# Kernel tuning notes

Measured on AMD Instinct MI355X. Metric: run time of the kernel, lower is better.

## Reference

```python
import jax, jax.numpy as jnp
import numpy as np

D_MODEL = 768
N_HEADS = 12
D_K = D_MODEL // N_HEADS


def setup_inputs() -> dict:
    key = jax.random.key(0)
    kq, kk, kv, kwq, kbq, kwo, kbo = jax.random.split(key, 7)
    B, S = 1, 4096
    s = 1.0 / np.sqrt(D_MODEL)
    return {
        "q": jax.random.normal(kq, (B, S, D_MODEL), jnp.float32),
        "k": jax.random.normal(kk, (B, S, D_MODEL), jnp.float32),
        "v": jax.random.normal(kv, (B, S, D_MODEL), jnp.float32),
        # nn.Linear weights stored as [out, in]; note the original forward
        # uses W_q for Q, K, AND V (W_k/W_v are never used), so only W_q and
        # W_o are materialized here.
        "Wq": jax.random.uniform(kwq, (D_MODEL, D_MODEL), jnp.float32, -s, s),
        "bq": jax.random.uniform(kbq, (D_MODEL,), jnp.float32, -s, s),
        "Wo": jax.random.uniform(kwo, (D_MODEL, D_MODEL), jnp.float32, -s, s),
        "bo": jax.random.uniform(kbo, (D_MODEL,), jnp.float32, -s, s),
    }


def _split_heads(x):  # [B,S,D] -> [B,H,S,Dk]
    B, S, _ = x.shape
    return x.reshape(B, S, N_HEADS, D_K).transpose(0, 2, 1, 3)


def reference(q, k, v, Wq, bq, Wo, bo):
    # Faithful to source: same W_q projection applied to q, k, v.
    Q = _split_heads(q @ Wq.T + bq)
    K = _split_heads(k @ Wq.T + bq)
    V = _split_heads(v @ Wq.T + bq)
    scale = 1.0 / np.sqrt(D_K).astype(np.float32)
    scores = jnp.einsum("bhqd,bhkd->bhqk", Q, K) * scale  # [B,H,S,S]
    probs = jax.nn.softmax(scores, axis=-1)
    atten = jnp.einsum("bhqk,bhkd->bhqd", probs, V)
    B, _, S, _ = atten.shape
    concat = atten.transpose(0, 2, 1, 3).reshape(B, S, D_MODEL)
    return concat @ Wo.T + bo
```

## Files before the change

### kernel.cpp

```cpp
#include <hip/hip_runtime.h>
#include <stdint.h>
#include <math.h>


#define SQ 4096
#define DM 768
#define NH 12

typedef float f32x4 __attribute__((ext_vector_type(4)));
typedef short bf16x8 __attribute__((ext_vector_type(8)));
typedef unsigned int u32x4 __attribute__((ext_vector_type(4)));
typedef unsigned short ushort_t;

static __device__ __forceinline__ ushort_t f2bf(float f) {
    unsigned int u = __builtin_bit_cast(unsigned int, f);
    u += 0x7fffu + ((u >> 16) & 1u);
    return (ushort_t)(u >> 16);
}

static __device__ __forceinline__ unsigned int cvt_pk_bf16(float a, float b) {
    unsigned int d;
    asm("v_cvt_pk_bf16_f32 %0, %1, %2" : "=v"(d) : "v"(a), "v"(b));
    return d;
}

static __device__ __forceinline__ float exp2_hw(float x) {
    float r;
    asm("v_exp_f32 %0, %1" : "=v"(r) : "v"(x));
    return r;
}

static __device__ __forceinline__ void gload16(const ushort_t* g, ushort_t* l) {
    __builtin_amdgcn_global_load_lds(
        reinterpret_cast<const __attribute__((address_space(1))) unsigned int*>(
            reinterpret_cast<uintptr_t>(g)),
        reinterpret_cast<__attribute__((address_space(3))) unsigned int*>(
            reinterpret_cast<uintptr_t>(l)),
        16, 0, 0);
}

#define WAITV8 do { asm volatile("s_waitcnt vmcnt(8)" ::: "memory"); \
                    __builtin_amdgcn_sched_barrier(0); } while (0)
#define WAITV0 do { asm volatile("s_waitcnt vmcnt(0)" ::: "memory"); \
                    __builtin_amdgcn_sched_barrier(0); } while (0)

__global__ __launch_bounds__(256) void cvt_all(
    const float* __restrict__ q, const float* __restrict__ k,
    const float* __restrict__ v, const float* __restrict__ Wq,
    const float* __restrict__ Wo, ushort_t* __restrict__ xb,
    ushort_t* __restrict__ wqb, ushort_t* __restrict__ wob) {
    const int NE4 = (SQ * DM) / 4;
    const int NW4 = (DM * DM) / 4;
    int i = blockIdx.x * 256 + threadIdx.x;
    const float* src;
    ushort_t* dst;
    if (i < NE4) { src = q; dst = xb; }
    else if (i < 2 * NE4) { src = k; dst = xb + SQ * DM; i -= NE4; }
    else if (i < 3 * NE4) { src = v; dst = xb + 2 * SQ * DM; i -= 2 * NE4; }
    else if (i < 3 * NE4 + NW4) { src = Wq; dst = wqb; i -= 3 * NE4; }
    else if (i < 3 * NE4 + 2 * NW4) { src = Wo; dst = wob; i -= 3 * NE4 + NW4; }
    else return;
    float4 x = reinterpret_cast<const float4*>(src)[i];
    ushort4 o;
    o.x = f2bf(x.x); o.y = f2bf(x.y); o.z = f2bf(x.z); o.w = f2bf(x.w);
    reinterpret_cast<ushort4*>(dst)[i] = o;
}

template <int EPI>
__global__ __launch_bounds__(256) void gemm_bf16(
    const ushort_t* __restrict__ A, const ushort_t* __restrict__ B,
    const float* __restrict__ bias, ushort_t* __restrict__ proj,
    ushort_t* __restrict__ vt, float* __restrict__ outf) {
    __shared__ __align__(16) ushort_t lsA[128 * 64];
    __shared__ __align__(16) ushort_t lsB[128 * 64];
    const int tid = threadIdx.x;
    const int lane = tid & 63;
    const int w = tid >> 6;
    const int wm = w >> 1, wn = w & 1;
    const int g = lane >> 4, li = lane & 15;
    const int NB = (EPI == 2) ? 32 : 6;
    const int bm = blockIdx.x / NB, bn = blockIdx.x % NB;
    const int arow = bm * 128, brow = bn * 128;
    const int sr = lane >> 3;
    const int sc = ((lane & 7) ^ sr) * 8;

    f32x4 acc[4][4] = {};

    for (int kt = 0; kt < 12; ++kt) {
        const int k0 = kt * 64;
        __syncthreads();
#pragma unroll
        for (int c = 0; c < 4; ++c) {
            const int chunk = w * 4 + c;
            const int r = chunk * 8 + sr;
            gload16(A + (size_t)(arow + r) * DM + k0 + sc, lsA + chunk * 512);
            gload16(B + (size_t)(brow + r) * DM + k0 + sc, lsB + chunk * 512);
        }
        __syncthreads();

        bf16x8 af[4][2];
#pragma unroll
        for (int mf = 0; mf < 4; ++mf) {
            const int row = wm * 64 + mf * 16 + li;
#pragma unroll
            for (int ks = 0; ks < 2; ++ks)
                af[mf][ks] = *reinterpret_cast<const bf16x8*>(
                    lsA + row * 64 + ((ks * 32 + g * 8) ^ ((li & 7) << 3)));
        }
#pragma unroll
        for (int nf = 0; nf < 4; ++nf) {
            const int row = wn * 64 + nf * 16 + li;
            bf16x8 b0 = *reinterpret_cast<const bf16x8*>(
                lsB + row * 64 + ((g * 8) ^ ((li & 7) << 3)));
            bf16x8 b1 = *reinterpret_cast<const bf16x8*>(
                lsB + row * 64 + ((32 + g * 8) ^ ((li & 7) << 3)));
#pragma unroll
            for (int mf = 0; mf < 4; ++mf) {
                acc[mf][nf] = __builtin_amdgcn_mfma_f32_16x16x32_bf16(af[mf][0], b0, acc[mf][nf], 0, 0, 0);
                acc[mf][nf] = __builtin_amdgcn_mfma_f32_16x16x32_bf16(af[mf][1], b1, acc[mf][nf], 0, 0, 0);
            }
        }
    }

    if (EPI == 0) {
        const float qscale = (arow < 4096) ? 0.18033688011112042f : 1.0f;
#pragma unroll
        for (int nf = 0; nf < 4; ++nf) {
            const int col = brow + wn * 64 + nf * 16 + li;
            const float bv = bias[col];
#pragma unroll
            for (int mf = 0; mf < 4; ++mf) {
                const int row0 = arow + wm * 64 + mf * 16 + g * 4;
#pragma unroll
                for (int r = 0; r < 4; ++r)
                    proj[(size_t)(row0 + r) * DM + col] = f2bf((acc[mf][nf][r] + bv) * qscale);
            }
        }
    } else if (EPI == 2) {
        float bv[4][4];
#pragma unroll
        for (int mf = 0; mf < 4; ++mf)
#pragma unroll
            for (int r = 0; r < 4; ++r)
                bv[mf][r] = bias[arow + wm * 64 + mf * 16 + g * 4 + r];
#pragma unroll
        for (int nf = 0; nf < 4; ++nf) {
            const int j = brow + wn * 64 + nf * 16 + li;
            const int pos = (j & ~31) | ((j & 0xC) << 1) | (((j >> 4) & 1) << 2) | (j & 3);
#pragma unroll
            for (int mf = 0; mf < 4; ++mf) {
                const int row0 = arow + wm * 64 + mf * 16 + g * 4;
#pragma unroll
                for (int r = 0; r < 4; ++r)
                    vt[(size_t)(row0 + r) * SQ + pos] = f2bf(acc[mf][nf][r] + bv[mf][r]);
            }
        }
    } else {
#pragma unroll
        for (int nf = 0; nf < 4; ++nf) {
            const int col = brow + wn * 64 + nf * 16 + li;
            const float bv = bias[col];
#pragma unroll
            for (int mf = 0; mf < 4; ++mf) {
                const int row0 = arow + wm * 64 + mf * 16 + g * 4;
#pragma unroll
                for (int r = 0; r < 4; ++r)
                    outf[(size_t)(row0 + r) * DM + col] = acc[mf][nf][r] + bv;
            }
        }
    }
}

__global__ __launch_bounds__(256) void attn_bf16(
    const ushort_t* __restrict__ qk, const ushort_t* __restrict__ vtb,
    ushort_t* __restrict__ cc) {
    __shared__ __align__(16) ushort_t smem[32768];

    const int tid = threadIdx.x, lane = tid & 63, w = tid >> 6;
    const int g = lane >> 4, li = lane & 15;
    const int logical = (blockIdx.x & 7) * 96 + (blockIdx.x >> 3);
    const int h = logical >> 6, qb = logical & 63;
    const int sr = lane >> 3;
    const int sc = ((lane & 7) ^ sr) * 8;
    const int vdr = lane >> 2;
    const int vsc = ((lane & 3) ^ ((lane >> 3) & 3)) * 8;

    const ushort_t* Kb = qk + (size_t)(4096 + w * 1024) * DM + (size_t)h * 64;
    const ushort_t* Vb = vtb + (size_t)(h * 64) * SQ + w * 1024;

    ushort_t* K0 = smem + w * 8192;
    ushort_t* V0 = K0 + 2048;
    ushort_t* K1 = K0 + 4096;
    ushort_t* V1 = K0 + 6144;

    bf16x8 qf[4][2];
#pragma unroll
    for (int qh = 0; qh < 4; ++qh)
#pragma unroll
        for (int ks = 0; ks < 2; ++ks)
            qf[qh][ks] = *reinterpret_cast<const bf16x8*>(
                qk + (size_t)(qb * 64 + qh * 16 + li) * DM + h * 64 + ks * 32 + g * 8);

    f32x4 oacc[4][5] = {};

    const unsigned int one2 = 0x3F803F80u;
    u32x4 onesu = {one2, one2, one2, one2};
    const bf16x8 vones = __builtin_bit_cast(bf16x8, onesu);

    WAITV0;

#pragma unroll
    for (int c = 0; c < 4; ++c) {
        gload16(Kb + (size_t)(c * 8 + sr) * DM + sc, K0 + c * 512);
        gload16(Vb + (size_t)(c * 16 + vdr) * SQ + vsc, V0 + c * 512);
    }

#define STEP(kp, vp, kn, vn, nxt, DOSTAGE)                                     \
    do {                                                                       \
        if (DOSTAGE) {                                                         \
            const int kvo = (nxt) * 32;                                        \
            _Pragma("unroll") for (int c = 0; c < 4; ++c) {                    \
                gload16(Kb + (size_t)(kvo + c * 8 + sr) * DM + sc,             \
                        (kn) + c * 512);                                       \
                gload16(Vb + (size_t)(c * 16 + vdr) * SQ + kvo + vsc,          \
                        (vn) + c * 512);                                       \
            }                                                                  \
            WAITV8;                                                            \
        } else {                                                               \
            WAITV0;                                                            \
        }                                                                      \
        f32x4 sf[4][2];                                                        \
        _Pragma("unroll") for (int qh = 0; qh < 4; ++qh)                       \
            _Pragma("unroll") for (int nf = 0; nf < 2; ++nf)                   \
                sf[qh][nf] = (f32x4){0.f, 0.f, 0.f, 0.f};                      \
        __builtin_amdgcn_s_setprio(1);                                         \
        _Pragma("unroll") for (int nf = 0; nf < 2; ++nf) {                     \
            const int row = nf * 16 + li;                                      \
            bf16x8 kb0 = *reinterpret_cast<const bf16x8*>(                     \
                (kp) + row * 64 + ((g * 8) ^ ((li & 7) << 3)));                \
            bf16x8 kb1 = *reinterpret_cast<const bf16x8*>(                     \
                (kp) + row * 64 + ((32 + g * 8) ^ ((li & 7) << 3)));           \
            _Pragma("unroll") for (int qh = 0; qh < 4; ++qh) {                 \
                sf[qh][nf] = __builtin_amdgcn_mfma_f32_16x16x32_bf16(          \
                    kb0, qf[qh][0], sf[qh][nf], 0, 0, 0);                      \
                sf[qh][nf] = __builtin_amdgcn_mfma_f32_16x16x32_bf16(          \
                    kb1, qf[qh][1], sf[qh][nf], 0, 0, 0);                      \
            }                                                                  \
        }                                                                      \
        __builtin_amdgcn_s_setprio(0);                                         \
        bf16x8 pa[4];                                                          \
        _Pragma("unroll") for (int qh = 0; qh < 4; ++qh) {                     \
            f32x4 p0, p1;                                                      \
            _Pragma("unroll") for (int r = 0; r < 4; ++r) {                    \
                p0[r] = exp2_hw(sf[qh][0][r]);                                 \
                p1[r] = exp2_hw(sf[qh][1][r]);                                 \
            }                                                                  \
            u32x4 pu;                                                          \
            pu.x = cvt_pk_bf16(p0[0], p0[1]);                                  \
            pu.y = cvt_pk_bf16(p0[2], p0[3]);                                  \
            pu.z = cvt_pk_bf16(p1[0], p1[1]);                                  \
            pu.w = cvt_pk_bf16(p1[2], p1[3]);                                  \
            pa[qh] = __builtin_bit_cast(bf16x8, pu);                           \
        }                                                                      \
        __builtin_amdgcn_s_setprio(1);                                         \
        _Pragma("unroll") for (int nv = 0; nv < 4; ++nv) {                     \
            const int vrow = nv * 16 + li;                                     \
            bf16x8 vb = *reinterpret_cast<const bf16x8*>(                      \
                (vp) + vrow * 32 + ((g ^ ((li >> 1) & 3)) * 8));               \
            _Pragma("unroll") for (int qh = 0; qh < 4; ++qh)                   \
                oacc[qh][nv] = __builtin_amdgcn_mfma_f32_16x16x32_bf16(        \
                    pa[qh], vb, oacc[qh][nv], 0, 0, 0);                        \
        }                                                                      \
        _Pragma("unroll") for (int qh = 0; qh < 4; ++qh)                       \
            oacc[qh][4] = __builtin_amdgcn_mfma_f32_16x16x32_bf16(             \
                pa[qh], vones, oacc[qh][4], 0, 0, 0);                          \
        __builtin_amdgcn_s_setprio(0);                                         \
    } while (0)

#pragma unroll 1
    for (int t = 0; t < 15; ++t) {
        STEP(K0, V0, K1, V1, 2 * t + 1, true);
        STEP(K1, V1, K0, V0, 2 * t + 2, true);
    }
    STEP(K0, V0, K1, V1, 31, true);
    STEP(K1, V1, K0, V0, 32, false);
#undef STEP

    __syncthreads();
    float* ob = reinterpret_cast<float*>(smem);
    if (w > 0) {
        float* base = ob + (w - 1) * 5120;
#pragma unroll
        for (int qh = 0; qh < 4; ++qh)
#pragma unroll
            for (int nv = 0; nv < 5; ++nv)
                *reinterpret_cast<f32x4*>(
                    base + ((qh * 5 + nv) * 64 + lane) * 4) = oacc[qh][nv];
    }
    __syncthreads();
    if (w == 0) {
#pragma unroll
        for (int j = 0; j < 3; ++j) {
            const float* base = ob + j * 5120;
#pragma unroll
            for (int qh = 0; qh < 4; ++qh)
#pragma unroll
                for (int nv = 0; nv < 5; ++nv)
                    oacc[qh][nv] += *reinterpret_cast<const f32x4*>(
                        base + ((qh * 5 + nv) * 64 + lane) * 4);
        }
#pragma unroll
        for (int qh = 0; qh < 4; ++qh) {
            float inv[4];
#pragma unroll
            for (int r = 0; r < 4; ++r) inv[r] = 1.0f / oacc[qh][4][r];
#pragma unroll
            for (int nv = 0; nv < 4; ++nv)
#pragma unroll
                for (int r = 0; r < 4; ++r) {
                    const int row = qb * 64 + qh * 16 + g * 4 + r;
                    const int col = h * 64 + nv * 16 + li;
                    cc[(size_t)row * DM + col] = f2bf(oacc[qh][nv][r] * inv[r]);
                }
        }
    }
}

extern "C" void kernel_launch(void* const* d_in, const int* in_sizes, int n_in,
                              void* d_out, int out_size, void* d_ws, size_t ws_size,
                              hipStream_t stream) {
    const float* q = (const float*)d_in[0];
    const float* k = (const float*)d_in[1];
    const float* v = (const float*)d_in[2];
    const float* Wq = (const float*)d_in[3];
    const float* bq = (const float*)d_in[4];
    const float* Wo = (const float*)d_in[5];
    const float* bo = (const float*)d_in[6];
    float* out = (float*)d_out;

    ushort_t* ws = (ushort_t*)d_ws;
    const int NE = SQ * DM;
    ushort_t* xb = ws;
    ushort_t* wqb = ws + 3 * NE;
    ushort_t* wob = wqb + DM * DM;
    ushort_t* proj = wob + DM * DM;
    ushort_t* vt = proj + 2 * NE;
    ushort_t* cc = vt + NE;

    const int n4 = 3 * (NE / 4) + 2 * ((DM * DM) / 4);
    cvt_all<<<(n4 + 255) / 256, 256, 0, stream>>>(q, k, v, Wq, Wo, xb, wqb, wob);

    gemm_bf16<0><<<(8192 / 128) * 6, 256, 0, stream>>>(xb, wqb, bq, proj, (ushort_t*)nullptr, (float*)nullptr);

    gemm_bf16<2><<<(768 / 128) * 32, 256, 0, stream>>>(wqb, xb + 2 * NE, bq, (ushort_t*)nullptr, vt, (float*)nullptr);

    attn_bf16<<<NH * (SQ / 64), 256, 0, stream>>>(proj, vt, cc);

    gemm_bf16<1><<<(SQ / 128) * 6, 256, 0, stream>>>(cc, wob, bo, (ushort_t*)nullptr, (ushort_t*)nullptr, out);
}
```

Before: 156.5 us.

## Triple-buffer attention KV stages, shrink LDS tiles, merge QK and V projection GEMMs

The attention kernel now stages 16-key K/V tiles into three rotating LDS buffers instead of 32-key tiles in two, splits waits into vmcnt(8)/vmcnt(4), and pairs two 16-key QK blocks per PV MFMA. V is stored with a simpler XOR layout and read as two short4 halves. LDS drops to 48KB with launch_bounds(256,3) so more blocks fit per CU, and the cross-wave reduction becomes a tree. The QK and V projection GEMMs are fused into one 576-block launch to cut a kernel launch. The risks are more register pressure, smaller tiles with more frequent waits, and subtle layout correctness.

```diff
diff --git a/kernel.cpp b/kernel.cpp
--- a/kernel.cpp
+++ b/kernel.cpp
@@ -10,7 +10,10 @@
 typedef float f32x4 __attribute__((ext_vector_type(4)));
 typedef short bf16x8 __attribute__((ext_vector_type(8)));
 typedef unsigned int u32x4 __attribute__((ext_vector_type(4)));
+typedef unsigned int u32x2 __attribute__((ext_vector_type(2)));
 typedef unsigned short ushort_t;
+
+#define MFMA32(a, b, c) __builtin_amdgcn_mfma_f32_16x16x32_bf16((a), (b), (c), 0, 0, 0)
 
 static __device__ __forceinline__ ushort_t f2bf(float f) {
     unsigned int u = __builtin_bit_cast(unsigned int, f);
@@ -41,8 +44,12 @@
 
 #define WAITV8 do { asm volatile("s_waitcnt vmcnt(8)" ::: "memory"); \
                     __builtin_amdgcn_sched_barrier(0); } while (0)
+#define WAITV4 do { asm volatile("s_waitcnt vmcnt(4)" ::: "memory"); \
+                    __builtin_amdgcn_sched_barrier(0); } while (0)
 #define WAITV0 do { asm volatile("s_waitcnt vmcnt(0)" ::: "memory"); \
                     __builtin_amdgcn_sched_barrier(0); } while (0)
+#define WAITLGKM0 do { asm volatile("s_waitcnt lgkmcnt(0)" ::: "memory"); \
+                       __builtin_amdgcn_sched_barrier(0); } while (0)
 
 __global__ __launch_bounds__(256) void cvt_all(
     const float* __restrict__ q, const float* __restrict__ k,
@@ -66,11 +73,10 @@
     reinterpret_cast<ushort4*>(dst)[i] = o;
 }
 
-template <int EPI>
-__global__ __launch_bounds__(256) void gemm_bf16(
-    const ushort_t* __restrict__ A, const ushort_t* __restrict__ B,
-    const float* __restrict__ bias, ushort_t* __restrict__ proj,
-    ushort_t* __restrict__ vt, float* __restrict__ outf) {
+__global__ __launch_bounds__(256) void gemm_qkv(
+    const ushort_t* __restrict__ xb, const ushort_t* __restrict__ wqb,
+    const float* __restrict__ bq, ushort_t* __restrict__ proj,
+    ushort_t* __restrict__ vt) {
     __shared__ __align__(16) ushort_t lsA[128 * 64];
     __shared__ __align__(16) ushort_t lsB[128 * 64];
     const int tid = threadIdx.x;
@@ -78,8 +84,18 @@
     const int w = tid >> 6;
     const int wm = w >> 1, wn = w & 1;
     const int g = lane >> 4, li = lane & 15;
-    const int NB = (EPI == 2) ? 32 : 6;
-    const int bm = blockIdx.x / NB, bn = blockIdx.x % NB;
+    const bool isV = blockIdx.x >= 384;
+    const ushort_t* A;
+    const ushort_t* B;
+    int bm, bn;
+    if (!isV) {
+        A = xb; B = wqb;
+        bm = blockIdx.x / 6; bn = blockIdx.x % 6;
+    } else {
+        A = wqb; B = xb + 2 * SQ * DM;
+        const int b2 = blockIdx.x - 384;
+        bm = b2 / 32; bn = b2 % 32;
+    }
     const int arow = bm * 128, brow = bn * 128;
     const int sr = lane >> 3;
     const int sc = ((lane & 7) ^ sr) * 8;
@@ -116,18 +132,18 @@
                 lsB + row * 64 + ((32 + g * 8) ^ ((li & 7) << 3)));
 #pragma unroll
             for (int mf = 0; mf < 4; ++mf) {
-                acc[mf][nf] = __builtin_amdgcn_mfma_f32_16x16x32_bf16(af[mf][0], b0, acc[mf][nf], 0, 0, 0);
-                acc[mf][nf] = __builtin_amdgcn_mfma_f32_16x16x32_bf16(af[mf][1], b1, acc[mf][nf], 0, 0, 0);
+                acc[mf][nf] = MFMA32(af[mf][0], b0, acc[mf][nf]);
+                acc[mf][nf] = MFMA32(af[mf][1], b1, acc[mf][nf]);
             }
         }
     }
 
-    if (EPI == 0) {
+    if (!isV) {
         const float qscale = (arow < 4096) ? 0.18033688011112042f : 1.0f;
 #pragma unroll
         for (int nf = 0; nf < 4; ++nf) {
             const int col = brow + wn * 64 + nf * 16 + li;
-            const float bv = bias[col];
+            const float bv = bq[col];
 #pragma unroll
             for (int mf = 0; mf < 4; ++mf) {
                 const int row0 = arow + wm * 64 + mf * 16 + g * 4;
@@ -136,17 +152,18 @@
                     proj[(size_t)(row0 + r) * DM + col] = f2bf((acc[mf][nf][r] + bv) * qscale);
             }
         }
-    } else if (EPI == 2) {
+    } else {
         float bv[4][4];
 #pragma unroll
         for (int mf = 0; mf < 4; ++mf)
 #pragma unroll
             for (int r = 0; r < 4; ++r)
-                bv[mf][r] = bias[arow + wm * 64 + mf * 16 + g * 4 + r];
+                bv[mf][r] = bq[arow + wm * 64 + mf * 16 + g * 4 + r];
+        const int xg = (g & 1) << 3;
 #pragma unroll
         for (int nf = 0; nf < 4; ++nf) {
             const int j = brow + wn * 64 + nf * 16 + li;
-            const int pos = (j & ~31) | ((j & 0xC) << 1) | (((j >> 4) & 1) << 2) | (j & 3);
+            const int pos = j ^ xg;
 #pragma unroll
             for (int mf = 0; mf < 4; ++mf) {
                 const int row0 = arow + wm * 64 + mf * 16 + g * 4;
@@ -155,26 +172,80 @@
                     vt[(size_t)(row0 + r) * SQ + pos] = f2bf(acc[mf][nf][r] + bv[mf][r]);
             }
         }
-    } else {
+    }
+}
+
+__global__ __launch_bounds__(256) void gemm_out(
+    const ushort_t* __restrict__ cc, const ushort_t* __restrict__ wob,
+    const float* __restrict__ bo, float* __restrict__ outf) {
+    __shared__ __align__(16) ushort_t lsA[128 * 64];
+    __shared__ __align__(16) ushort_t lsB[128 * 64];
+    const int tid = threadIdx.x;
+    const int lane = tid & 63;
+    const int w = tid >> 6;
+    const int wm = w >> 1, wn = w & 1;
+    const int g = lane >> 4, li = lane & 15;
+    const int bm = blockIdx.x / 6, bn = blockIdx.x % 6;
+    const int arow = bm * 128, brow = bn * 128;
+    const int sr = lane >> 3;
+    const int sc = ((lane & 7) ^ sr) * 8;
+
+    f32x4 acc[4][4] = {};
+
+    for (int kt = 0; kt < 12; ++kt) {
+        const int k0 = kt * 64;
+        __syncthreads();
+#pragma unroll
+        for (int c = 0; c < 4; ++c) {
+            const int chunk = w * 4 + c;
+            const int r = chunk * 8 + sr;
+            gload16(cc + (size_t)(arow + r) * DM + k0 + sc, lsA + chunk * 512);
+            gload16(wob + (size_t)(brow + r) * DM + k0 + sc, lsB + chunk * 512);
+        }
+        __syncthreads();
+
+        bf16x8 af[4][2];
+#pragma unroll
+        for (int mf = 0; mf < 4; ++mf) {
+            const int row = wm * 64 + mf * 16 + li;
+#pragma unroll
+            for (int ks = 0; ks < 2; ++ks)
+                af[mf][ks] = *reinterpret_cast<const bf16x8*>(
+                    lsA + row * 64 + ((ks * 32 + g * 8) ^ ((li & 7) << 3)));
+        }
 #pragma unroll
         for (int nf = 0; nf < 4; ++nf) {
-            const int col = brow + wn * 64 + nf * 16 + li;
-            const float bv = bias[col];
+            const int row = wn * 64 + nf * 16 + li;
+            bf16x8 b0 = *reinterpret_cast<const bf16x8*>(
+                lsB + row * 64 + ((g * 8) ^ ((li & 7) << 3)));
+            bf16x8 b1 = *reinterpret_cast<const bf16x8*>(
+                lsB + row * 64 + ((32 + g * 8) ^ ((li & 7) << 3)));
 #pragma unroll
             for (int mf = 0; mf < 4; ++mf) {
-                const int row0 = arow + wm * 64 + mf * 16 + g * 4;
-#pragma unroll
-                for (int r = 0; r < 4; ++r)
-                    outf[(size_t)(row0 + r) * DM + col] = acc[mf][nf][r] + bv;
+                acc[mf][nf] = MFMA32(af[mf][0], b0, acc[mf][nf]);
+                acc[mf][nf] = MFMA32(af[mf][1], b1, acc[mf][nf]);
             }
         }
     }
-}
-
-__global__ __launch_bounds__(256) void attn_bf16(
+
+#pragma unroll
+    for (int nf = 0; nf < 4; ++nf) {
+        const int col = brow + wn * 64 + nf * 16 + li;
+        const float bv = bo[col];
+#pragma unroll
+        for (int mf = 0; mf < 4; ++mf) {
+            const int row0 = arow + wm * 64 + mf * 16 + g * 4;
+#pragma unroll
+            for (int r = 0; r < 4; ++r)
+                outf[(size_t)(row0 + r) * DM + col] = acc[mf][nf][r] + bv;
+        }
+    }
+}
+
+__global__ __launch_bounds__(256, 3) void attn_bf16(
     const ushort_t* __restrict__ qk, const ushort_t* __restrict__ vtb,
     ushort_t* __restrict__ cc) {
-    __shared__ __align__(16) ushort_t smem[32768];
+    __shared__ __align__(16) ushort_t smem[24576];
 
     const int tid = threadIdx.x, lane = tid & 63, w = tid >> 6;
     const int g = lane >> 4, li = lane & 15;
@@ -182,16 +253,19 @@
     const int h = logical >> 6, qb = logical & 63;
     const int sr = lane >> 3;
     const int sc = ((lane & 7) ^ sr) * 8;
-    const int vdr = lane >> 2;
-    const int vsc = ((lane & 3) ^ ((lane >> 3) & 3)) * 8;
+    const int vd = lane >> 1, vh = lane & 1;
 
     const ushort_t* Kb = qk + (size_t)(4096 + w * 1024) * DM + (size_t)h * 64;
     const ushort_t* Vb = vtb + (size_t)(h * 64) * SQ + w * 1024;
 
-    ushort_t* K0 = smem + w * 8192;
-    ushort_t* V0 = K0 + 2048;
-    ushort_t* K1 = K0 + 4096;
-    ushort_t* V1 = K0 + 6144;
+    ushort_t* base = smem + w * 6144;
+    ushort_t* K0 = base;          ushort_t* V0 = base + 1024;
+    ushort_t* K1 = base + 2048;   ushort_t* V1 = base + 3072;
+    ushort_t* K2 = base + 4096;   ushort_t* V2 = base + 5120;
+
+    const int ko0 = li * 64 + ((g * 8) ^ ((li & 7) << 3));
+    const int ko1 = li * 64 + ((32 + g * 8) ^ ((li & 7) << 3));
+    const int vo = li * 16 + 4 * (g ^ (((li >> 2) & 1) << 1));
 
     bf16x8 qf[4][2];
 #pragma unroll
@@ -202,113 +276,160 @@
                 qk + (size_t)(qb * 64 + qh * 16 + li) * DM + h * 64 + ks * 32 + g * 8);
 
     f32x4 oacc[4][5] = {};
+    u32x2 paA[4];
 
     const unsigned int one2 = 0x3F803F80u;
     u32x4 onesu = {one2, one2, one2, one2};
     const bf16x8 vones = __builtin_bit_cast(bf16x8, onesu);
 
+    auto stage = [&](ushort_t* KT, ushort_t* VT, int kvo) {
+        gload16(Kb + (size_t)(kvo + sr) * DM + sc, KT);
+        gload16(Kb + (size_t)(kvo + 8 + sr) * DM + sc, KT + 512);
+        gload16(Vb + (size_t)vd * SQ + kvo + vh * 8, VT);
+        gload16(Vb + (size_t)(32 + vd) * SQ + kvo + vh * 8, VT + 512);
+    };
+
+    auto qkexp = [&](const ushort_t* KT, f32x4* P) {
+        bf16x8 kb0 = *reinterpret_cast<const bf16x8*>(KT + ko0);
+        bf16x8 kb1 = *reinterpret_cast<const bf16x8*>(KT + ko1);
+        __builtin_amdgcn_s_setprio(1);
+#pragma unroll
+        for (int qh = 0; qh < 4; ++qh) {
+            f32x4 s = {};
+            s = MFMA32(kb0, qf[qh][0], s);
+            s = MFMA32(kb1, qf[qh][1], s);
+            P[qh] = s;
+        }
+        __builtin_amdgcn_s_setprio(0);
+#pragma unroll
+        for (int qh = 0; qh < 4; ++qh) {
+            f32x4 p;
+#pragma unroll
+            for (int r = 0; r < 4; ++r) p[r] = exp2_hw(P[qh][r]);
+            P[qh] = p;
+        }
+    };
+
+    auto pvacc = [&](const ushort_t* VA, const ushort_t* VB, const bf16x8* pa) {
+        __builtin_amdgcn_s_setprio(1);
+#pragma unroll
+        for (int nv = 0; nv < 4; ++nv) {
+            short4 a4 = *reinterpret_cast<const short4*>(VA + vo + nv * 256);
+            short4 b4 = *reinterpret_cast<const short4*>(VB + vo + nv * 256);
+            bf16x8 vb = {a4.x, a4.y, a4.z, a4.w, b4.x, b4.y, b4.z, b4.w};
+#pragma unroll
+            for (int qh = 0; qh < 4; ++qh)
+                oacc[qh][nv] = MFMA32(pa[qh], vb, oacc[qh][nv]);
+        }
+#pragma unroll
+        for (int qh = 0; qh < 4; ++qh)
+            oacc[qh][4] = MFMA32(pa[qh], vones, oacc[qh][4]);
+        __builtin_amdgcn_s_setprio(0);
+    };
+
+    auto packA = [&](const f32x4* P) {
+#pragma unroll
+        for (int qh = 0; qh < 4; ++qh) {
+            u32x2 u;
+            u.x = cvt_pk_bf16(P[qh][0], P[qh][1]);
+            u.y = cvt_pk_bf16(P[qh][2], P[qh][3]);
+            paA[qh] = u;
+        }
+    };
+
+    auto packO = [&](const f32x4* P, bf16x8* pa) {
+#pragma unroll
+        for (int qh = 0; qh < 4; ++qh) {
+            u32x4 pu;
+            pu.x = paA[qh].x;
+            pu.y = paA[qh].y;
+            pu.z = cvt_pk_bf16(P[qh][0], P[qh][1]);
+            pu.w = cvt_pk_bf16(P[qh][2], P[qh][3]);
+            pa[qh] = __builtin_bit_cast(bf16x8, pu);
+        }
+    };
+
+    auto pair_full = [&](ushort_t* KE, ushort_t* VE, ushort_t* KO, ushort_t* VO,
+                         ushort_t* KS1, ushort_t* VS1, ushort_t* KS2,
+                         ushort_t* VS2, int e) {
+        stage(KS1, VS1, (e + 2) * 16);
+        WAITV8;
+        f32x4 P[4];
+        qkexp(KE, P);
+        packA(P);
+        WAITV4;
+        f32x4 P2[4];
+        qkexp(KO, P2);
+        bf16x8 pa[4];
+        packO(P2, pa);
+        pvacc(VE, VO, pa);
+        WAITLGKM0;
+        stage(KS2, VS2, (e + 3) * 16);
+    };
+
     WAITV0;
-
-#pragma unroll
-    for (int c = 0; c < 4; ++c) {
-        gload16(Kb + (size_t)(c * 8 + sr) * DM + sc, K0 + c * 512);
-        gload16(Vb + (size_t)(c * 16 + vdr) * SQ + vsc, V0 + c * 512);
-    }
-
-#define STEP(kp, vp, kn, vn, nxt, DOSTAGE)                                     \
-    do {                                                                       \
-        if (DOSTAGE) {                                                         \
-            const int kvo = (nxt) * 32;                                        \
-            _Pragma("unroll") for (int c = 0; c < 4; ++c) {                    \
-                gload16(Kb + (size_t)(kvo + c * 8 + sr) * DM + sc,             \
-                        (kn) + c * 512);                                       \
-                gload16(Vb + (size_t)(c * 16 + vdr) * SQ + kvo + vsc,          \
-                        (vn) + c * 512);                                       \
-            }                                                                  \
-            WAITV8;                                                            \
-        } else {                                                               \
-            WAITV0;                                                            \
-        }                                                                      \
-        f32x4 sf[4][2];                                                        \
-        _Pragma("unroll") for (int qh = 0; qh < 4; ++qh)                       \
-            _Pragma("unroll") for (int nf = 0; nf < 2; ++nf)                   \
-                sf[qh][nf] = (f32x4){0.f, 0.f, 0.f, 0.f};                      \
-        __builtin_amdgcn_s_setprio(1);                                         \
-        _Pragma("unroll") for (int nf = 0; nf < 2; ++nf) {                     \
-            const int row = nf * 16 + li;                                      \
-            bf16x8 kb0 = *reinterpret_cast<const bf16x8*>(                     \
-                (kp) + row * 64 + ((g * 8) ^ ((li & 7) << 3)));                \
-            bf16x8 kb1 = *reinterpret_cast<const bf16x8*>(                     \
-                (kp) + row * 64 + ((32 + g * 8) ^ ((li & 7) << 3)));           \
-            _Pragma("unroll") for (int qh = 0; qh < 4; ++qh) {                 \
-                sf[qh][nf] = __builtin_amdgcn_mfma_f32_16x16x32_bf16(          \
-                    kb0, qf[qh][0], sf[qh][nf], 0, 0, 0);                      \
-                sf[qh][nf] = __builtin_amdgcn_mfma_f32_16x16x32_bf16(          \
-                    kb1, qf[qh][1], sf[qh][nf], 0, 0, 0);                      \
-            }                                                                  \
-        }                                                                      \
-        __builtin_amdgcn_s_setprio(0);                                         \
-        bf16x8 pa[4];                                                          \
-        _Pragma("unroll") for (int qh = 0; qh < 4; ++qh) {                     \
-            f32x4 p0, p1;                                                      \
-            _Pragma("unroll") for (int r = 0; r < 4; ++r) {                    \
-                p0[r] = exp2_hw(sf[qh][0][r]);                                 \
-                p1[r] = exp2_hw(sf[qh][1][r]);                                 \
-            }                                                                  \
-            u32x4 pu;                                                          \
-            pu.x = cvt_pk_bf16(p0[0], p0[1]);                                  \
-            pu.y = cvt_pk_bf16(p0[2], p0[3]);                                  \
-            pu.z = cvt_pk_bf16(p1[0], p1[1]);                                  \
-            pu.w = cvt_pk_bf16(p1[2], p1[3]);                                  \
-            pa[qh] = __builtin_bit_cast(bf16x8, pu);                           \
-        }                                                                      \
-        __builtin_amdgcn_s_setprio(1);                                         \
-        _Pragma("unroll") for (int nv = 0; nv < 4; ++nv) {                     \
-            const int vrow = nv * 16 + li;                                     \
-            bf16x8 vb = *reinterpret_cast<const bf16x8*>(                      \
-                (vp) + vrow * 32 + ((g ^ ((li >> 1) & 3)) * 8));               \
-            _Pragma("unroll") for (int qh = 0; qh < 4; ++qh)                   \
-                oacc[qh][nv] = __builtin_amdgcn_mfma_f32_16x16x32_bf16(        \
-                    pa[qh], vb, oacc[qh][nv], 0, 0, 0);                        \
-        }                                                                      \
-        _Pragma("unroll") for (int qh = 0; qh < 4; ++qh)                       \
-            oacc[qh][4] = __builtin_amdgcn_mfma_f32_16x16x32_bf16(             \
-                pa[qh], vones, oacc[qh][4], 0, 0, 0);                          \
-        __builtin_amdgcn_s_setprio(0);                                         \
-    } while (0)
+    stage(K0, V0, 0);
+    stage(K1, V1, 16);
 
 #pragma unroll 1
-    for (int t = 0; t < 15; ++t) {
-        STEP(K0, V0, K1, V1, 2 * t + 1, true);
-        STEP(K1, V1, K0, V0, 2 * t + 2, true);
-    }
-    STEP(K0, V0, K1, V1, 31, true);
-    STEP(K1, V1, K0, V0, 32, false);
-#undef STEP
+    for (int i = 0; i < 10; ++i) {
+        const int e = i * 6;
+        pair_full(K0, V0, K1, V1, K2, V2, K0, V0, e);
+        pair_full(K2, V2, K0, V0, K1, V1, K2, V2, e + 2);
+        pair_full(K1, V1, K2, V2, K0, V0, K1, V1, e + 4);
+    }
+    pair_full(K0, V0, K1, V1, K2, V2, K0, V0, 60);
+    {
+        WAITV4;
+        f32x4 P[4];
+        qkexp(K2, P);
+        packA(P);
+        WAITV0;
+        f32x4 P2[4];
+        qkexp(K0, P2);
+        bf16x8 pa[4];
+        packO(P2, pa);
+        pvacc(V2, V0, pa);
+    }
 
     __syncthreads();
     float* ob = reinterpret_cast<float*>(smem);
-    if (w > 0) {
-        float* base = ob + (w - 1) * 5120;
+    if (w >= 2) {
+        float* bse = ob + (w - 2) * 5120;
 #pragma unroll
         for (int qh = 0; qh < 4; ++qh)
 #pragma unroll
             for (int nv = 0; nv < 5; ++nv)
                 *reinterpret_cast<f32x4*>(
-                    base + ((qh * 5 + nv) * 64 + lane) * 4) = oacc[qh][nv];
+                    bse + ((qh * 5 + nv) * 64 + lane) * 4) = oacc[qh][nv];
+    }
+    __syncthreads();
+    if (w < 2) {
+        const float* bse = ob + w * 5120;
+#pragma unroll
+        for (int qh = 0; qh < 4; ++qh)
+#pragma unroll
+            for (int nv = 0; nv < 5; ++nv)
+                oacc[qh][nv] += *reinterpret_cast<const f32x4*>(
+                    bse + ((qh * 5 + nv) * 64 + lane) * 4);
+    }
+    __syncthreads();
+    if (w == 1) {
+#pragma unroll
+        for (int qh = 0; qh < 4; ++qh)
+#pragma unroll
+            for (int nv = 0; nv < 5; ++nv)
+                *reinterpret_cast<f32x4*>(
+                    ob + ((qh * 5 + nv) * 64 + lane) * 4) = oacc[qh][nv];
     }
     __syncthreads();
     if (w == 0) {
 #pragma unroll
-        for (int j = 0; j < 3; ++j) {
-            const float* base = ob + j * 5120;
-#pragma unroll
-            for (int qh = 0; qh < 4; ++qh)
-#pragma unroll
-                for (int nv = 0; nv < 5; ++nv)
-                    oacc[qh][nv] += *reinterpret_cast<const f32x4*>(
-                        base + ((qh * 5 + nv) * 64 + lane) * 4);
-        }
+        for (int qh = 0; qh < 4; ++qh)
+#pragma unroll
+            for (int nv = 0; nv < 5; ++nv)
+                oacc[qh][nv] += *reinterpret_cast<const f32x4*>(
+                    ob + ((qh * 5 + nv) * 64 + lane) * 4);
 #pragma unroll
         for (int qh = 0; qh < 4; ++qh) {
             float inv[4];
@@ -350,11 +471,9 @@
     const int n4 = 3 * (NE / 4) + 2 * ((DM * DM) / 4);
     cvt_all<<<(n4 + 255) / 256, 256, 0, stream>>>(q, k, v, Wq, Wo, xb, wqb, wob);
 
-    gemm_bf16<0><<<(8192 / 128) * 6, 256, 0, stream>>>(xb, wqb, bq, proj, (ushort_t*)nullptr, (float*)nullptr);
-
-    gemm_bf16<2><<<(768 / 128) * 32, 256, 0, stream>>>(wqb, xb + 2 * NE, bq, (ushort_t*)nullptr, vt, (float*)nullptr);
+    gemm_qkv<<<576, 256, 0, stream>>>(xb, wqb, bq, proj, vt);
 
     attn_bf16<<<NH * (SQ / 64), 256, 0, stream>>>(proj, vt, cc);
 
-    gemm_bf16<1><<<(SQ / 128) * 6, 256, 0, stream>>>(cc, wob, bo, (ushort_t*)nullptr, (ushort_t*)nullptr, out);
-}
+    gemm_out<<<(SQ / 128) * 6, 256, 0, stream>>>(cc, wob, bo, out);
+}
```

Result: faster. 140.5 us (-10.2%).
